# Optimization experiments

Hardware: AMD Instinct MI355X
Metric: run time of the kernel (lower is better)

Reference implementation:

```python
import jax, jax.numpy as jnp
import numpy as np

B, S, C, H = 2, 512, 25, 768


def setup_inputs() -> dict:
    key = jax.random.key(0)
    ks = jax.random.split(key, 10)
    sc = 1.0 / np.sqrt(H)
    return {
        "token_rep": jax.random.normal(ks[0], (B, S, H), jnp.float32),
        "label_rep": jax.random.normal(ks[1], (B, C, H), jnp.float32),
        # proj_token: Linear(H, 2H) stored as [in, out] for x @ W
        "Wt": jax.random.normal(ks[2], (H, 2 * H), jnp.float32) * sc,
        "bt": jnp.zeros((2 * H,), jnp.float32),
        # proj_label: Linear(H, 2H)
        "Wl": jax.random.normal(ks[3], (H, 2 * H), jnp.float32) * sc,
        "bl": jnp.zeros((2 * H,), jnp.float32),
        # out_mlp[0]: Linear(3H, 4H)
        "W1": jax.random.normal(ks[4], (3 * H, 4 * H), jnp.float32) * (1.0 / np.sqrt(3 * H)),
        "b1": jnp.zeros((4 * H,), jnp.float32),
        # out_mlp[3]: Linear(4H, 3)
        "W2": jax.random.normal(ks[5], (4 * H, 3), jnp.float32) * (1.0 / np.sqrt(4 * H)),
        "b2": jnp.zeros((3,), jnp.float32),
    }


def reference(token_rep, label_rep, Wt, bt, Wl, bl, W1, b1, W2, b2):
    h = token_rep.shape[-1]
    # project and split into (additive half, multiplicative half)
    tp = token_rep @ Wt + bt            # [B,S,2H]
    lp = label_rep @ Wl + bl            # [B,C,2H]
    ta, tb = tp[..., :h], tp[..., h:]
    la, lb = lp[..., :h], lp[..., h:]
    # First MLP layer on concat([ta, la, tb*lb]) without materializing the concat:
    # split W1 row-wise into the three input blocks.
    W1t, W1l, W1p = W1[:h], W1[h:2 * h], W1[2 * h:]
    hid = (ta @ W1t)[:, :, None, :] \
        + (la @ W1l)[:, None, :, :] \
        + jnp.einsum('bsh,bch,hf->bscf', tb, lb, W1p) \
        + b1                            # [B,S,C,4H]
    # Dropout is identity in eval mode.
    return jax.nn.relu(hid) @ W2 + b2   # [B,S,C,3]
```

## Files before the change

kernel.cpp:

```cpp
#include <hip/hip_runtime.h>
#include <hip/hip_bf16.h>
#include <cstdint>
#include <cstddef>

#define BB 2
#define SS 512
#define CC 25
#define HH 768
#define H2 1536
#define H3 2304
#define H4 3072
#define XC_STRIDE ((size_t)96 * 512 * 8)

typedef __attribute__((ext_vector_type(8))) short bf16x8;
typedef __attribute__((ext_vector_type(4))) float f32x4;

#define DEVINL static __device__ __forceinline__

DEVINL unsigned short f2bf(float f) {
  union { float f; unsigned u; } v; v.f = f;
  unsigned r = v.u + 0x7FFF + ((v.u >> 16) & 1);
  return (unsigned short)(r >> 16);
}
DEVINL float bf2f(unsigned short b) {
  union { unsigned u; float f; } v; v.u = ((unsigned)b) << 16; return v.f;
}

DEVINL void async16(const void* g, void* l) {
  __builtin_amdgcn_global_load_lds(
      (const __attribute__((address_space(1))) void*)g,
      (__attribute__((address_space(3))) void*)l, 16, 0, 0);
}

__global__ void k_prep(const float* __restrict__ token,
                       const float* __restrict__ label,
                       const float* __restrict__ b2,
                       const float* __restrict__ Wt,
                       const float* __restrict__ Wl,
                       const float* __restrict__ W1,
                       unsigned short* __restrict__ TC,
                       unsigned short* __restrict__ LC,
                       float* __restrict__ out,
                       unsigned short* __restrict__ WtC,
                       unsigned short* __restrict__ WlC,
                       unsigned short* __restrict__ W1C) {
  __shared__ float tile[64][33];
  const int bid = blockIdx.x;
  const int tid = threadIdx.x;
  if (bid < 408) {
    const float* in;
    unsigned short* o;
    int R, RP, kt, rt;
    if (bid < 384) {
      in = token; o = TC; R = 1024; RP = 1024; kt = bid % 24; rt = bid / 24;
    } else {
      in = label; o = LC; R = 50; RP = 64; kt = bid - 384; rt = 0;
    }
    const int k0 = kt * 32, r0 = rt * 64;
    const int tx = tid & 31, ty = tid >> 5;
#pragma unroll
    for (int i = 0; i < 8; i++) {
      int r = r0 + ty + i * 8;
      tile[ty + i * 8][tx] = in[(size_t)min(r, R - 1) * HH + k0 + tx];
    }
    __syncthreads();
    const int rl = tid & 63, kcl = tid >> 6;
    bf16x8 ov;
#pragma unroll
    for (int j = 0; j < 8; j++) ov[j] = (short)f2bf(tile[rl][kcl * 8 + j]);
    *(bf16x8*)&o[((size_t)((k0 >> 3) + kcl) * RP + r0 + rl) * 8] = ov;
  } else if (bid < 708) {
    int i = (bid - 408) * 256 + tid;
    if (i < BB * SS * CC * 3) out[i] = b2[i % 3];
  } else {
    const int wb = bid - 708;
    const float* in;
    unsigned short* o;
    int N, bx, by;
    if (wb < 3456) {
      in = W1; o = W1C; N = H4; bx = wb % 48; by = wb / 48;
    } else if (wb < 4032) {
      int b = wb - 3456; in = Wt; o = WtC; N = H2; bx = b % 24; by = b / 24;
    } else {
      int b = wb - 4032; in = Wl; o = WlC; N = H2; bx = b % 24; by = b / 24;
    }
    const int f = bx * 64 + (tid & 63);
    const int hc = by * 4 + (tid >> 6);
    bf16x8 ov;
#pragma unroll
    for (int j = 0; j < 8; j++)
      ov[j] = (short)f2bf(in[(size_t)(hc * 8 + j) * N + f]);
    *(bf16x8*)&o[((size_t)hc * N + f) * 8] = ov;
  }
}

DEVINL void mm_kloop(const unsigned short* __restrict__ Ab, int NRA, int MA,
                     int m0, const unsigned short* __restrict__ Bt, int NRB,
                     int n0, unsigned short* As, unsigned short* Bs,
                     f32x4 (&acc)[4][4]) {
  const int tid = threadIdx.x;
  const int lane = tid & 63;
  const int wave = tid >> 6;
  const int q = lane >> 4;
  const int li = lane & 15;
  const int wm = (wave >> 1) * 64;
  const int wn = (wave & 1) * 64;

  int sr[4], skc[4], sra[4];
#pragma unroll
  for (int j = 0; j < 4; j++) {
    int slot = j * 256 + tid;
    skc[j] = slot >> 7;
    sr[j] = slot & 127;
    sra[j] = min(m0 + sr[j], MA - 1);
  }
  auto stage = [&](int kciter) {
#pragma unroll
    for (int j = 0; j < 4; j++) {
      int slot = j * 256 + tid;
      async16(Ab + ((size_t)(kciter + skc[j]) * NRA + sra[j]) * 8,
              (char*)As + slot * 16);
      async16(Bt + ((size_t)(kciter + skc[j]) * NRB + n0 + sr[j]) * 8,
              (char*)Bs + slot * 16);
    }
  };

  stage(0);
  for (int it = 0; it < 12; it++) {
    __syncthreads();
#pragma unroll
    for (int ks = 0; ks < 2; ks++) {
      bf16x8 af[4], bb[4];
#pragma unroll
      for (int mi = 0; mi < 4; mi++)
        af[mi] = *(const bf16x8*)&As[((ks * 4 + q) * 128 + wm + mi * 16 + li) * 8];
#pragma unroll
      for (int ni = 0; ni < 4; ni++)
        bb[ni] = *(const bf16x8*)&Bs[((ks * 4 + q) * 128 + wn + ni * 16 + li) * 8];
#pragma unroll
      for (int mi = 0; mi < 4; mi++)
#pragma unroll
        for (int ni = 0; ni < 4; ni++)
          acc[mi][ni] = __builtin_amdgcn_mfma_f32_16x16x32_bf16(
              af[mi], bb[ni], acc[mi][ni], 0, 0, 0);
    }
    __syncthreads();
    if (it + 1 < 12) stage((it + 1) * 8);
  }
}

__global__ __launch_bounds__(256, 4) void k_mm1(
    const unsigned short* __restrict__ TC, const unsigned short* __restrict__ LC,
    const unsigned short* __restrict__ WtC, const unsigned short* __restrict__ WlC,
    const float* __restrict__ bt, const float* __restrict__ bl,
    unsigned short* __restrict__ TP, unsigned short* __restrict__ LP) {
  __shared__ __align__(16) unsigned short As[8 * 128 * 8];
  __shared__ __align__(16) unsigned short Bs[8 * 128 * 8];
  const int bid = blockIdx.x;
  const int nt = bid % 12, my = bid / 12;
  const bool tok = my < 8;
  const unsigned short* A = tok ? TC : LC;
  const unsigned short* Bt = tok ? WtC : WlC;
  const float* bias = tok ? bt : bl;
  unsigned short* C = tok ? TP : LP;
  const int NRA = tok ? 1024 : 64, MA = tok ? 1024 : 50;
  const int m0 = tok ? my * 128 : 0;
  const int ldc = NRA;
  const int n0 = nt * 128;

  f32x4 acc[4][4];
#pragma unroll
  for (int i = 0; i < 4; i++)
#pragma unroll
    for (int j = 0; j < 4; j++) acc[i][j] = (f32x4){0.f, 0.f, 0.f, 0.f};
  mm_kloop(A, NRA, MA, m0, Bt, H2, n0, As, Bs, acc);

  const int lane = threadIdx.x & 63, wave = threadIdx.x >> 6;
  const int q = lane >> 4, li = lane & 15;
  const int wm = (wave >> 1) * 64, wn = (wave & 1) * 64;
#pragma unroll
  for (int mi = 0; mi < 4; mi++)
#pragma unroll
    for (int rr = 0; rr < 4; rr++) {
      int row = m0 + wm + mi * 16 + q * 4 + rr;
      if (row < MA) {
#pragma unroll
        for (int ni = 0; ni < 4; ni++) {
          int col = n0 + wn + ni * 16 + li;
          C[((size_t)(col >> 3) * ldc + row) * 8 + (col & 7)] =
              f2bf(acc[mi][ni][rr] + bias[col]);
        }
      }
    }
}

__global__ __launch_bounds__(256, 4) void k_mm2(
    const unsigned short* __restrict__ TP, const unsigned short* __restrict__ LP,
    const unsigned short* __restrict__ W1C,
    float* __restrict__ base, float* __restrict__ al,
    unsigned short* __restrict__ XC) {
  __shared__ __align__(16) unsigned short As[8 * 128 * 8];
  __shared__ __align__(16) unsigned short Bs[8 * 128 * 8];
  const int bid = blockIdx.x;
  if (bid < 216) {
    const int nt = bid % 24, my = bid / 24;
    const bool tok = my < 8;
    const unsigned short* A = tok ? TP : LP;
    const unsigned short* Bt = tok ? W1C : W1C + (size_t)96 * H4 * 8;
    float* Cf = tok ? base : al;
    const int NRA = tok ? 1024 : 64, MA = tok ? 1024 : 50;
    const int m0 = tok ? my * 128 : 0;
    const int n0 = nt * 128;

    f32x4 acc[4][4];
#pragma unroll
    for (int i = 0; i < 4; i++)
#pragma unroll
      for (int j = 0; j < 4; j++) acc[i][j] = (f32x4){0.f, 0.f, 0.f, 0.f};
    mm_kloop(A, NRA, MA, m0, Bt, H4, n0, As, Bs, acc);

    const int lane = threadIdx.x & 63, wave = threadIdx.x >> 6;
    const int q = lane >> 4, li = lane & 15;
    const int wm = (wave >> 1) * 64, wn = (wave & 1) * 64;
#pragma unroll
    for (int mi = 0; mi < 4; mi++)
#pragma unroll
      for (int rr = 0; rr < 4; rr++) {
        int row = m0 + wm + mi * 16 + q * 4 + rr;
        if (row < MA) {
#pragma unroll
          for (int ni = 0; ni < 4; ni++) {
            int col = n0 + wn + ni * 16 + li;
            Cf[(size_t)row * H4 + col] = acc[mi][ni][rr];
          }
        }
      }
  } else {
    const int i = bid - 216;
    const int bc = i / 192;
    const int rem = i % 192;
    const int hc = rem >> 1;
    const int s = (rem & 1) * 256 + threadIdx.x;
    const int b = bc / CC;
    bf16x8 tv = *(const bf16x8*)&TP[((size_t)(96 + hc) * 1024 + b * 512 + s) * 8];
    bf16x8 lv = *(const bf16x8*)&LP[((size_t)(96 + hc) * 64 + bc) * 8];
    bf16x8 o;
#pragma unroll
    for (int j = 0; j < 8; j++)
      o[j] = (short)f2bf(bf2f((unsigned short)tv[j]) * bf2f((unsigned short)lv[j]));
    *(bf16x8*)&XC[(size_t)bc * XC_STRIDE + ((size_t)hc * 512 + s) * 8] = o;
  }
}

__global__ __launch_bounds__(512, 2) void k_scorer(
    const unsigned short* __restrict__ XC,
    const unsigned short* __restrict__ Bt,
    const float* __restrict__ base, const float* __restrict__ al,
    const float* __restrict__ b1, const float* __restrict__ W2,
    float* __restrict__ out) {
  __shared__ __align__(16) unsigned short As[3][4 * 256 * 8];
  __shared__ __align__(16) unsigned short Bs[3][4 * 256 * 8];
  const int tid = threadIdx.x;
  const int lane = tid & 63;
  const int wave = tid >> 6;
  const int q = lane >> 4;
  const int li = lane & 15;
  const int wm = (wave >> 2) * 128;
  const int wn = (wave & 3) * 64;

  const int n0 = blockIdx.x * 256;
  const int bc = blockIdx.y >> 1;
  const int m0 = (blockIdx.y & 1) * 256;
  const unsigned short* Ab = XC + (size_t)bc * XC_STRIDE;

  int skc[2], srow[2];
#pragma unroll
  for (int j = 0; j < 2; j++) {
    int slot = j * 512 + tid;
    skc[j] = slot >> 8;
    srow[j] = slot & 255;
  }
  auto stage = [&](int t, int bufsel) {
    const int kc0 = t * 4;
#pragma unroll
    for (int j = 0; j < 2; j++) {
      int slot = j * 512 + tid;
      async16(Ab + ((size_t)(kc0 + skc[j]) * 512 + m0 + srow[j]) * 8,
              (char*)&As[bufsel][0] + slot * 16);
    }
#pragma unroll
    for (int j = 0; j < 2; j++) {
      int slot = j * 512 + tid;
      async16(Bt + ((size_t)(kc0 + skc[j]) * 3072 + n0 + srow[j]) * 8,
              (char*)&Bs[bufsel][0] + slot * 16);
    }
  };

  f32x4 acc[8][4];
#pragma unroll
  for (int i = 0; i < 8; i++)
#pragma unroll
    for (int j = 0; j < 4; j++) acc[i][j] = (f32x4){0.f, 0.f, 0.f, 0.f};

  stage(0, 0);
  stage(1, 1);
  asm volatile("s_waitcnt vmcnt(4)" ::: "memory");
  __builtin_amdgcn_s_barrier();
  asm volatile("" ::: "memory");

  int c0 = 0, c1 = 1, c2 = 2;
  const int abase = (q * 256 + wm + li) * 8;
  const int bbase = (q * 256 + wn + li) * 8;
  for (int v = 0; v < 24; v++) {
    if (v + 2 < 24) stage(v + 2, c2);

    const unsigned short* Ap = &As[c0][0];
    const unsigned short* Bp = &Bs[c0][0];
    bf16x8 af[8], bb[4];
#pragma unroll
    for (int mi = 0; mi < 8; mi++)
      af[mi] = *(const bf16x8*)&Ap[abase + mi * 16 * 8];
#pragma unroll
    for (int ni = 0; ni < 4; ni++)
      bb[ni] = *(const bf16x8*)&Bp[bbase + ni * 16 * 8];
    __builtin_amdgcn_s_setprio(1);
#pragma unroll
    for (int mi = 0; mi < 8; mi++)
#pragma unroll
      for (int ni = 0; ni < 4; ni++)
        acc[mi][ni] = __builtin_amdgcn_mfma_f32_16x16x32_bf16(
            af[mi], bb[ni], acc[mi][ni], 0, 0, 0);
    __builtin_amdgcn_s_setprio(0);

    if (v < 23) {
      if (v < 22)
        asm volatile("s_waitcnt vmcnt(4) lgkmcnt(0)" ::: "memory");
      else
        asm volatile("s_waitcnt vmcnt(0) lgkmcnt(0)" ::: "memory");
      __builtin_amdgcn_s_barrier();
      asm volatile("" ::: "memory");
    }
    int tmp = c0; c0 = c1; c1 = c2; c2 = tmp;
  }

  const int b = bc / CC, c = bc % CC;
  int fcol[4];
  float alb[4];
#pragma unroll
  for (int ni = 0; ni < 4; ni++) {
    int f = n0 + wn + ni * 16 + li;
    fcol[ni] = f;
    alb[ni] = al[(size_t)bc * H4 + f] + b1[f];
  }
  bf16x8 w2f[2];
#pragma unroll
  for (int ks = 0; ks < 2; ks++)
#pragma unroll
    for (int jj = 0; jj < 8; jj++) {
      int f = n0 + wn + ks * 32 + q * 8 + jj;
      float v = (li < 3) ? W2[(size_t)f * 3 + li] : 0.f;
      w2f[ks][jj] = (short)f2bf(v);
    }
  unsigned short* Ew = (unsigned short*)((char*)As + wave * 2304);

#pragma unroll
  for (int mi = 0; mi < 8; mi++) {
    float bs[4][4];
#pragma unroll
    for (int rr = 0; rr < 4; rr++) {
      int s_l = m0 + wm + mi * 16 + q * 4 + rr;
      const float* bp = base + (size_t)(b * SS + s_l) * H4;
#pragma unroll
      for (int ni = 0; ni < 4; ni++) bs[ni][rr] = bp[fcol[ni]];
    }
#pragma unroll
    for (int rr = 0; rr < 4; rr++)
#pragma unroll
      for (int ni = 0; ni < 4; ni++) {
        float v = acc[mi][ni][rr] + bs[ni][rr] + alb[ni];
        v = fmaxf(v, 0.f);
        Ew[(q * 4 + rr) * 72 + ni * 16 + li] = f2bf(v);
      }
    f32x4 oc = (f32x4){0.f, 0.f, 0.f, 0.f};
#pragma unroll
    for (int ks = 0; ks < 2; ks++) {
      bf16x8 ef = *(const bf16x8*)&Ew[li * 72 + ks * 32 + q * 8];
      oc = __builtin_amdgcn_mfma_f32_16x16x32_bf16(ef, w2f[ks], oc, 0, 0, 0);
    }
#pragma unroll
    for (int rr = 0; rr < 4; rr++) {
      int s_l = m0 + wm + mi * 16 + q * 4 + rr;
      if (li < 3)
        atomicAdd(&out[((size_t)(b * SS + s_l) * CC + c) * 3 + li], oc[rr]);
    }
  }
}


extern "C" void kernel_launch(void* const* d_in, const int* in_sizes, int n_in,
                              void* d_out, int out_size, void* d_ws, size_t ws_size,
                              hipStream_t stream) {
  (void)in_sizes; (void)n_in; (void)ws_size; (void)out_size;
  const float* token = (const float*)d_in[0];
  const float* label = (const float*)d_in[1];
  const float* Wt    = (const float*)d_in[2];
  const float* bt    = (const float*)d_in[3];
  const float* Wl    = (const float*)d_in[4];
  const float* bl    = (const float*)d_in[5];
  const float* W1    = (const float*)d_in[6];
  const float* b1    = (const float*)d_in[7];
  const float* W2    = (const float*)d_in[8];
  const float* b2    = (const float*)d_in[9];
  float* out = (float*)d_out;

  char* p = (char*)d_ws;
  auto alloc = [&](size_t bytes) {
    char* r = p;
    p += (bytes + 255) & ~(size_t)255;
    return r;
  };
  unsigned short* TC  = (unsigned short*)alloc((size_t)96 * 1024 * 8 * 2);
  unsigned short* LC  = (unsigned short*)alloc((size_t)96 * 64 * 8 * 2);
  unsigned short* WtC = (unsigned short*)alloc((size_t)96 * 1536 * 8 * 2);
  unsigned short* WlC = (unsigned short*)alloc((size_t)96 * 1536 * 8 * 2);
  unsigned short* W1C = (unsigned short*)alloc((size_t)288 * 3072 * 8 * 2);
  unsigned short* TP  = (unsigned short*)alloc((size_t)192 * 1024 * 8 * 2);
  unsigned short* LP  = (unsigned short*)alloc((size_t)192 * 64 * 8 * 2);
  unsigned short* XC  = (unsigned short*)alloc((size_t)CC * BB * XC_STRIDE * 2);
  float* base = (float*)alloc((size_t)BB * SS * H4 * 4);
  float* al   = (float*)alloc((size_t)BB * CC * H4 * 4);

  k_prep<<<5316, 256, 0, stream>>>(token, label, b2, Wt, Wl, W1,
                                   TC, LC, out, WtC, WlC, W1C);
  k_mm1<<<108, 256, 0, stream>>>(TC, LC, WtC, WlC, bt, bl, TP, LP);
  k_mm2<<<9816, 256, 0, stream>>>(TP, LP, W1C, base, al, XC);
  k_scorer<<<dim3(12, 100), 512, 0, stream>>>(
      XC, W1C + (size_t)192 * H4 * 8, base, al, b1, W2, out);
}
```

Baseline: 334.4 us.

## Restructure scorer GEMM into ping-pong double buffer with interleaved staged loads

Replaces the three-slot K-chunk ring in the scorer kernel with two larger buffers, each holding two K-chunks, and splits every tile into four MFMA phases separated by barriers. Async loads for the next tile are issued in slices between these phases. The aim is to spread global-to-LDS traffic across the compute and keep the MFMA units busier with prioritised bursts. The cost is many more barriers per tile, and the timing of the vmcnt waits must stay correct for the buffer reuse to be safe.

```diff
diff --git a/kernel.cpp b/kernel.cpp
--- a/kernel.cpp
+++ b/kernel.cpp
@@ -31,6 +31,11 @@
       (const __attribute__((address_space(1))) void*)g,
       (__attribute__((address_space(3))) void*)l, 16, 0, 0);
 }
+
+#define BAR() do { asm volatile("" ::: "memory"); \
+                   __builtin_amdgcn_s_barrier();  \
+                   asm volatile("" ::: "memory"); } while (0)
+#define MFMA16(a, b, c) __builtin_amdgcn_mfma_f32_16x16x32_bf16(a, b, c, 0, 0, 0)
 
 __global__ void k_prep(const float* __restrict__ token,
                        const float* __restrict__ label,
@@ -141,8 +146,7 @@
       for (int mi = 0; mi < 4; mi++)
 #pragma unroll
         for (int ni = 0; ni < 4; ni++)
-          acc[mi][ni] = __builtin_amdgcn_mfma_f32_16x16x32_bf16(
-              af[mi], bb[ni], acc[mi][ni], 0, 0, 0);
+          acc[mi][ni] = MFMA16(af[mi], bb[ni], acc[mi][ni]);
     }
     __syncthreads();
     if (it + 1 < 12) stage((it + 1) * 8);
@@ -258,8 +262,8 @@
     const float* __restrict__ base, const float* __restrict__ al,
     const float* __restrict__ b1, const float* __restrict__ W2,
     float* __restrict__ out) {
-  __shared__ __align__(16) unsigned short As[3][4 * 256 * 8];
-  __shared__ __align__(16) unsigned short Bs[3][4 * 256 * 8];
+  __shared__ __align__(16) unsigned short As[2][8 * 256 * 8];
+  __shared__ __align__(16) unsigned short Bs[2][8 * 256 * 8];
   const int tid = threadIdx.x;
   const int lane = tid & 63;
   const int wave = tid >> 6;
@@ -273,26 +277,26 @@
   const int m0 = (blockIdx.y & 1) * 256;
   const unsigned short* Ab = XC + (size_t)bc * XC_STRIDE;
 
-  int skc[2], srow[2];
-#pragma unroll
-  for (int j = 0; j < 2; j++) {
-    int slot = j * 512 + tid;
-    skc[j] = slot >> 8;
-    srow[j] = slot & 255;
-  }
-  auto stage = [&](int t, int bufsel) {
-    const int kc0 = t * 4;
+  auto stageA = [&](int t, int h) {
+    const int kcb = t * 8 + h * 4;
+    unsigned short* dst = &As[t & 1][h * 4 * 256 * 8];
 #pragma unroll
     for (int j = 0; j < 2; j++) {
       int slot = j * 512 + tid;
-      async16(Ab + ((size_t)(kc0 + skc[j]) * 512 + m0 + srow[j]) * 8,
-              (char*)&As[bufsel][0] + slot * 16);
-    }
+      int kcl = slot >> 8, r = slot & 255;
+      async16(Ab + ((size_t)(kcb + kcl) * 512 + m0 + r) * 8,
+              (char*)dst + slot * 16);
+    }
+  };
+  auto stageB = [&](int t, int h) {
+    const int kcb = t * 8 + h * 4;
+    unsigned short* dst = &Bs[t & 1][h * 4 * 256 * 8];
 #pragma unroll
     for (int j = 0; j < 2; j++) {
       int slot = j * 512 + tid;
-      async16(Bt + ((size_t)(kc0 + skc[j]) * 3072 + n0 + srow[j]) * 8,
-              (char*)&Bs[bufsel][0] + slot * 16);
+      int kcl = slot >> 8, r = slot & 255;
+      async16(Bt + ((size_t)(kcb + kcl) * 3072 + n0 + r) * 8,
+              (char*)dst + slot * 16);
     }
   };
 
@@ -302,45 +306,77 @@
 #pragma unroll
     for (int j = 0; j < 4; j++) acc[i][j] = (f32x4){0.f, 0.f, 0.f, 0.f};
 
-  stage(0, 0);
-  stage(1, 1);
+  stageA(0, 0); stageB(0, 0); stageA(0, 1); stageB(0, 1);
   asm volatile("s_waitcnt vmcnt(4)" ::: "memory");
-  __builtin_amdgcn_s_barrier();
-  asm volatile("" ::: "memory");
-
-  int c0 = 0, c1 = 1, c2 = 2;
-  const int abase = (q * 256 + wm + li) * 8;
-  const int bbase = (q * 256 + wn + li) * 8;
-  for (int v = 0; v < 24; v++) {
-    if (v + 2 < 24) stage(v + 2, c2);
-
-    const unsigned short* Ap = &As[c0][0];
-    const unsigned short* Bp = &Bs[c0][0];
-    bf16x8 af[8], bb[4];
+  BAR();
+
+  bf16x8 af[8], bb[4];
+  auto do_tile = [&](int t, const unsigned short* Ad, const unsigned short* Bd) {
+    const bool iss = (t + 1 < 12);
 #pragma unroll
     for (int mi = 0; mi < 8; mi++)
-      af[mi] = *(const bf16x8*)&Ap[abase + mi * 16 * 8];
-#pragma unroll
-    for (int ni = 0; ni < 4; ni++)
-      bb[ni] = *(const bf16x8*)&Bp[bbase + ni * 16 * 8];
+      af[mi] = *(const bf16x8*)&Ad[((0 + q) * 256 + wm + mi * 16 + li) * 8];
+    bb[0] = *(const bf16x8*)&Bd[((0 + q) * 256 + wn + 0 * 16 + li) * 8];
+    bb[1] = *(const bf16x8*)&Bd[((0 + q) * 256 + wn + 1 * 16 + li) * 8];
+    if (iss) stageA(t + 1, 0);
+    BAR();
     __builtin_amdgcn_s_setprio(1);
 #pragma unroll
+    for (int mi = 0; mi < 8; mi++) {
+      acc[mi][0] = MFMA16(af[mi], bb[0], acc[mi][0]);
+      acc[mi][1] = MFMA16(af[mi], bb[1], acc[mi][1]);
+    }
+    __builtin_amdgcn_s_setprio(0);
+    BAR();
+    bb[2] = *(const bf16x8*)&Bd[((0 + q) * 256 + wn + 2 * 16 + li) * 8];
+    bb[3] = *(const bf16x8*)&Bd[((0 + q) * 256 + wn + 3 * 16 + li) * 8];
+    if (iss) stageB(t + 1, 0);
+    BAR();
+    __builtin_amdgcn_s_setprio(1);
+#pragma unroll
+    for (int mi = 0; mi < 8; mi++) {
+      acc[mi][2] = MFMA16(af[mi], bb[2], acc[mi][2]);
+      acc[mi][3] = MFMA16(af[mi], bb[3], acc[mi][3]);
+    }
+    __builtin_amdgcn_s_setprio(0);
+    if (iss) { asm volatile("s_waitcnt vmcnt(4)" ::: "memory"); }
+    else     { asm volatile("s_waitcnt vmcnt(0)" ::: "memory"); }
+    BAR();
+#pragma unroll
     for (int mi = 0; mi < 8; mi++)
-#pragma unroll
-      for (int ni = 0; ni < 4; ni++)
-        acc[mi][ni] = __builtin_amdgcn_mfma_f32_16x16x32_bf16(
-            af[mi], bb[ni], acc[mi][ni], 0, 0, 0);
+      af[mi] = *(const bf16x8*)&Ad[((4 + q) * 256 + wm + mi * 16 + li) * 8];
+    bb[0] = *(const bf16x8*)&Bd[((4 + q) * 256 + wn + 0 * 16 + li) * 8];
+    bb[1] = *(const bf16x8*)&Bd[((4 + q) * 256 + wn + 1 * 16 + li) * 8];
+    if (iss) stageA(t + 1, 1);
+    BAR();
+    __builtin_amdgcn_s_setprio(1);
+#pragma unroll
+    for (int mi = 0; mi < 8; mi++) {
+      acc[mi][0] = MFMA16(af[mi], bb[0], acc[mi][0]);
+      acc[mi][1] = MFMA16(af[mi], bb[1], acc[mi][1]);
+    }
     __builtin_amdgcn_s_setprio(0);
-
-    if (v < 23) {
-      if (v < 22)
-        asm volatile("s_waitcnt vmcnt(4) lgkmcnt(0)" ::: "memory");
-      else
-        asm volatile("s_waitcnt vmcnt(0) lgkmcnt(0)" ::: "memory");
-      __builtin_amdgcn_s_barrier();
-      asm volatile("" ::: "memory");
-    }
-    int tmp = c0; c0 = c1; c1 = c2; c2 = tmp;
+    BAR();
+    bb[2] = *(const bf16x8*)&Bd[((4 + q) * 256 + wn + 2 * 16 + li) * 8];
+    bb[3] = *(const bf16x8*)&Bd[((4 + q) * 256 + wn + 3 * 16 + li) * 8];
+    if (iss) stageB(t + 1, 1);
+    BAR();
+    __builtin_amdgcn_s_setprio(1);
+#pragma unroll
+    for (int mi = 0; mi < 8; mi++) {
+      acc[mi][2] = MFMA16(af[mi], bb[2], acc[mi][2]);
+      acc[mi][3] = MFMA16(af[mi], bb[3], acc[mi][3]);
+    }
+    __builtin_amdgcn_s_setprio(0);
+    if (iss) { asm volatile("s_waitcnt vmcnt(4)" ::: "memory"); }
+    else     { asm volatile("s_waitcnt vmcnt(0)" ::: "memory"); }
+    BAR();
+  };
+
+#pragma unroll 1
+  for (int tt = 0; tt < 6; tt++) {
+    do_tile(2 * tt,     &As[0][0], &Bs[0][0]);
+    do_tile(2 * tt + 1, &As[1][0], &Bs[1][0]);
   }
 
   const int b = bc / CC, c = bc % CC;
@@ -361,23 +397,23 @@
       float v = (li < 3) ? W2[(size_t)f * 3 + li] : 0.f;
       w2f[ks][jj] = (short)f2bf(v);
     }
-  unsigned short* Ew = (unsigned short*)((char*)As + wave * 2304);
+  unsigned short* Ew = &As[0][0] + wave * 1152;
 
 #pragma unroll
   for (int mi = 0; mi < 8; mi++) {
-    float bs[4][4];
+    float bsv[4][4];
 #pragma unroll
     for (int rr = 0; rr < 4; rr++) {
       int s_l = m0 + wm + mi * 16 + q * 4 + rr;
       const float* bp = base + (size_t)(b * SS + s_l) * H4;
 #pragma unroll
-      for (int ni = 0; ni < 4; ni++) bs[ni][rr] = bp[fcol[ni]];
+      for (int ni = 0; ni < 4; ni++) bsv[ni][rr] = bp[fcol[ni]];
     }
 #pragma unroll
     for (int rr = 0; rr < 4; rr++)
 #pragma unroll
       for (int ni = 0; ni < 4; ni++) {
-        float v = acc[mi][ni][rr] + bs[ni][rr] + alb[ni];
+        float v = acc[mi][ni][rr] + bsv[ni][rr] + alb[ni];
         v = fmaxf(v, 0.f);
         Ew[(q * 4 + rr) * 72 + ni * 16 + li] = f2bf(v);
       }
@@ -385,7 +421,7 @@
 #pragma unroll
     for (int ks = 0; ks < 2; ks++) {
       bf16x8 ef = *(const bf16x8*)&Ew[li * 72 + ks * 32 + q * 8];
-      oc = __builtin_amdgcn_mfma_f32_16x16x32_bf16(ef, w2f[ks], oc, 0, 0, 0);
+      oc = MFMA16(ef, w2f[ks], oc);
     }
 #pragma unroll
     for (int rr = 0; rr < 4; rr++) {
```

Measured after the change: 449.3 us. 34.4% more time.
